# Optimization experiments

Measured on AMD Instinct MI355X. Metric: run time of the kernel, lower is better.

Reference implementation:

```python
import jax, jax.numpy as jnp
import numpy as np

SCALE = 0.1  # FullAttention(0.1) binds scale positionally

def setup_inputs() -> dict:
    key = jax.random.key(0)
    k1, k2, k3, k4, k5 = jax.random.split(key, 5)
    B, H, L, E = 128, 16, 64, 128
    C = H * E  # in_channel = 2048
    return {
        "queries": jax.random.normal(k1, (B, H, L, E), dtype=jnp.float32),
        "keys": jax.random.normal(k2, (B, H, L, E), dtype=jnp.float32),
        "values": jax.random.normal(k3, (B, H, L, E), dtype=jnp.float32),
        "W": jax.random.normal(k4, (C, C), dtype=jnp.float32) * (1.0 / np.sqrt(C)),
        "b": jax.random.normal(k5, (C,), dtype=jnp.float32) * 0.01,
    }

def reference(queries, keys, values, W, b):
    # inputs are [B, H, L, E]; module permutes to [B, L, H, E]
    q = jnp.transpose(queries, (0, 2, 1, 3))  # blhe
    k = jnp.transpose(keys, (0, 2, 1, 3))     # bshe
    v = jnp.transpose(values, (0, 2, 1, 3))   # bshd
    scores = jnp.einsum('blhe,bshe->bhls', q, k)
    A = jax.nn.softmax(SCALE * scores, axis=-1)  # dropout is identity in eval
    V = jnp.einsum('bhls,bshd->blhd', A, v)
    B_, L, H, D = V.shape
    out = V.reshape(-1, 64, H * D)  # view(-1, 64, in_channel)
    return out @ W.T + b
```

## Files before the change

### kernel.cpp

```cpp
#include <hip/hip_runtime.h>
#include <hip/hip_bf16.h>
#include <stdint.h>

typedef __bf16 bf16_t;
typedef __bf16 bf16x4 __attribute__((ext_vector_type(4)));
typedef __bf16 bf16x8 __attribute__((ext_vector_type(8)));
typedef float  f32x4  __attribute__((ext_vector_type(4)));

#define AS1 __attribute__((address_space(1)))
#define AS3 __attribute__((address_space(3)))

__device__ __forceinline__ void gld_lds16(const void* gp, void* lp) {
    __builtin_amdgcn_global_load_lds((const AS1 unsigned int*)gp,
                                     (AS3 unsigned int*)lp, 16, 0, 0);
}

__device__ __forceinline__ bf16_t bhi(float v) { return (bf16_t)v; }
__device__ __forceinline__ bf16_t blo(float v) {
    return (bf16_t)(v - (float)((bf16_t)v));
}

__global__ __launch_bounds__(256) void wconv_kernel(const float* __restrict__ W,
                                                    bf16_t* __restrict__ Wb) {
    const int i = (blockIdx.x * 256 + threadIdx.x) * 4;
    const float4 f = *(const float4*)&W[i];
    bf16x4 v = { (bf16_t)f.x, (bf16_t)f.y, (bf16_t)f.z, (bf16_t)f.w };
    *(bf16x4*)&Wb[i] = v;
}

#define QK_LD 136
#define VT_LD 72
#define SF_LD 65

__global__ __launch_bounds__(256) void attn_kernel(const float* __restrict__ Q,
                                                   const float* __restrict__ K,
                                                   const float* __restrict__ V,
                                                   bf16_t* __restrict__ X) {
    __shared__ __align__(16) char smem[53248];
    bf16_t* Qs = (bf16_t*)smem;
    bf16_t* Ks = (bf16_t*)(smem + 17408);
    bf16_t* Vt = (bf16_t*)(smem + 34816);
    float*  Sf = (float*)smem;
    bf16_t* Ps = (bf16_t*)(smem + 17408);
    bf16_t* Ob = (bf16_t*)smem;

    const int bh   = blockIdx.x;
    const int b    = bh >> 4;
    const int h    = bh & 15;
    const int t    = threadIdx.x;
    const int w    = t >> 6;
    const int lane = t & 63;
    const int row16 = lane & 15;
    const int quad  = lane >> 4;

    const float* Qg = Q + (size_t)bh * 8192;
    const float* Kg = K + (size_t)bh * 8192;
    const float* Vg = V + (size_t)bh * 8192;

    const int r  = t >> 2;
    const int c0 = (t & 3) * 32;

    float qv[32], kv[32];
#pragma unroll
    for (int j = 0; j < 8; ++j) {
        const int c = c0 + 4 * j;
        *(float4*)&qv[4 * j] = *(const float4*)&Qg[r * 128 + c];
        *(float4*)&kv[4 * j] = *(const float4*)&Kg[r * 128 + c];
        const float4 v4 = *(const float4*)&Vg[r * 128 + c];
        Vt[(c + 0) * VT_LD + r] = (bf16_t)v4.x;
        Vt[(c + 1) * VT_LD + r] = (bf16_t)v4.y;
        Vt[(c + 2) * VT_LD + r] = (bf16_t)v4.z;
        Vt[(c + 3) * VT_LD + r] = (bf16_t)v4.w;
    }

#define STAGE(slot, vals, CONV)                                            \
    {                                                                      \
        _Pragma("unroll")                                                  \
        for (int j = 0; j < 8; ++j) {                                      \
            const int c = c0 + 4 * j;                                      \
            bf16x4 o = { CONV(vals[4*j+0]), CONV(vals[4*j+1]),             \
                         CONV(vals[4*j+2]), CONV(vals[4*j+3]) };           \
            *(bf16x4*)&slot[r * QK_LD + c] = o;                            \
        }                                                                  \
    }

    f32x4 accS[4];
#pragma unroll
    for (int ni = 0; ni < 4; ++ni) accS[ni] = (f32x4){0.f, 0.f, 0.f, 0.f};

#define SCORE_PASS()                                                       \
    {                                                                      \
        _Pragma("unroll")                                                  \
        for (int kb = 0; kb < 4; ++kb) {                                   \
            const bf16x8 a = *(const bf16x8*)&Qs[(16*w + row16)*QK_LD + 32*kb + 8*quad]; \
            _Pragma("unroll")                                              \
            for (int ni = 0; ni < 4; ++ni) {                               \
                const bf16x8 bb = *(const bf16x8*)&Ks[(16*ni + row16)*QK_LD + 32*kb + 8*quad]; \
                accS[ni] = __builtin_amdgcn_mfma_f32_16x16x32_bf16(a, bb, accS[ni], 0, 0, 0); \
            }                                                              \
        }                                                                  \
    }

    STAGE(Qs, qv, bhi)
    STAGE(Ks, kv, blo)
    __syncthreads();
    SCORE_PASS()
    __syncthreads();
    STAGE(Ks, kv, bhi)
    __syncthreads();
    SCORE_PASS()
    __syncthreads();
    STAGE(Qs, qv, blo)
    __syncthreads();
    SCORE_PASS()
    __syncthreads();

#pragma unroll
    for (int ni = 0; ni < 4; ++ni)
#pragma unroll
        for (int rr = 0; rr < 4; ++rr)
            Sf[(16 * w + 4 * quad + rr) * SF_LD + 16 * ni + row16] = accS[ni][rr];
    __syncthreads();

    {
        const int c16 = (t & 3) * 16;
        float x[16];
        float mx = -1e30f;
#pragma unroll
        for (int j = 0; j < 16; ++j) {
            x[j] = Sf[r * SF_LD + c16 + j] * 0.1f;
            mx = fmaxf(mx, x[j]);
        }
        mx = fmaxf(mx, __shfl_xor(mx, 1));
        mx = fmaxf(mx, __shfl_xor(mx, 2));
        float sum = 0.f;
#pragma unroll
        for (int j = 0; j < 16; ++j) {
            x[j] = exp2f((x[j] - mx) * 1.44269504088896f);
            sum += x[j];
        }
        sum += __shfl_xor(sum, 1);
        sum += __shfl_xor(sum, 2);
        const float inv = 1.0f / sum;
#pragma unroll
        for (int j4 = 0; j4 < 4; ++j4) {
            bf16x4 p = { (bf16_t)(x[4 * j4 + 0] * inv), (bf16_t)(x[4 * j4 + 1] * inv),
                         (bf16_t)(x[4 * j4 + 2] * inv), (bf16_t)(x[4 * j4 + 3] * inv) };
            *(bf16x4*)&Ps[r * VT_LD + c16 + 4 * j4] = p;
        }
    }
    __syncthreads();

    f32x4 accO[8];
#pragma unroll
    for (int ni = 0; ni < 8; ++ni) accO[ni] = (f32x4){0.f, 0.f, 0.f, 0.f};
#pragma unroll
    for (int kb = 0; kb < 2; ++kb) {
        const bf16x8 a = *(const bf16x8*)&Ps[(16 * w + row16) * VT_LD + 32 * kb + 8 * quad];
#pragma unroll
        for (int ni = 0; ni < 8; ++ni) {
            const bf16x8 bb = *(const bf16x8*)&Vt[(16 * ni + row16) * VT_LD + 32 * kb + 8 * quad];
            accO[ni] = __builtin_amdgcn_mfma_f32_16x16x32_bf16(a, bb, accO[ni], 0, 0, 0);
        }
    }

#pragma unroll
    for (int ni = 0; ni < 8; ++ni)
#pragma unroll
        for (int rr = 0; rr < 4; ++rr)
            Ob[(16 * w + 4 * quad + rr) * QK_LD + 16 * ni + row16] = (bf16_t)accO[ni][rr];
    __syncthreads();

    {
        bf16_t* Xrow = X + (size_t)b * 64 * 2048 + h * 128 + (size_t)r * 2048;
#pragma unroll
        for (int j = 0; j < 4; ++j) {
            *(bf16x8*)&Xrow[c0 + 8 * j] = *(const bf16x8*)&Ob[r * QK_LD + c0 + 8 * j];
        }
    }
}

__global__ __launch_bounds__(256, 4) void gemm_kernel(const bf16_t* __restrict__ X,
                                                      const bf16_t* __restrict__ Wb,
                                                      const float* __restrict__ bias,
                                                      float* __restrict__ out) {
    __shared__ bf16_t As[128 * 64];
    __shared__ bf16_t Bs[128 * 64];

    const int t    = threadIdx.x;
    const int w    = t >> 6;
    const int lane = t & 63;
    const int row16 = lane & 15;
    const int quad  = lane >> 4;
    const int m0 = blockIdx.x * 128;
    const int n0 = blockIdx.y * 128;
    const int wm = w >> 1;
    const int wn = w & 1;

    const int row8 = lane >> 3;
    const int scol = 8 * ((lane & 7) ^ (row8 & 7));
    const bf16_t* gA = X  + (size_t)(m0 + 32 * w + row8) * 2048 + scol;
    const bf16_t* gB = Wb + (size_t)(n0 + 32 * w + row8) * 2048 + scol;
    bf16_t* lA = &As[(32 * w) * 64];
    bf16_t* lB = &Bs[(32 * w) * 64];

    const int sw = row16 & 7;
    int aoff[4][2], boff[4][2];
#pragma unroll
    for (int mi = 0; mi < 4; ++mi)
#pragma unroll
        for (int kk = 0; kk < 2; ++kk) {
            const int ar = 64 * wm + 16 * mi + row16;
            const int br = 64 * wn + 16 * mi + row16;
            aoff[mi][kk] = ar * 64 + 8 * ((4 * kk + quad) ^ sw);
            boff[mi][kk] = br * 64 + 8 * ((4 * kk + quad) ^ sw);
        }

    f32x4 acc[4][4];
#pragma unroll
    for (int mi = 0; mi < 4; ++mi)
#pragma unroll
        for (int ni = 0; ni < 4; ++ni) acc[mi][ni] = (f32x4){0.f, 0.f, 0.f, 0.f};

    for (int kb = 0; kb < 32; ++kb) {
        const int k0 = kb * 64;
        __syncthreads();
#pragma unroll
        for (int i = 0; i < 4; ++i) {
            gld_lds16(gA + (size_t)(8 * i) * 2048 + k0, lA + (8 * i) * 64);
            gld_lds16(gB + (size_t)(8 * i) * 2048 + k0, lB + (8 * i) * 64);
        }
        __syncthreads();

#pragma unroll
        for (int kk = 0; kk < 2; ++kk) {
            bf16x8 a[4], bb[4];
#pragma unroll
            for (int mi = 0; mi < 4; ++mi) a[mi]  = *(const bf16x8*)&As[aoff[mi][kk]];
#pragma unroll
            for (int ni = 0; ni < 4; ++ni) bb[ni] = *(const bf16x8*)&Bs[boff[ni][kk]];
#pragma unroll
            for (int mi = 0; mi < 4; ++mi)
#pragma unroll
                for (int ni = 0; ni < 4; ++ni)
                    acc[mi][ni] = __builtin_amdgcn_mfma_f32_16x16x32_bf16(a[mi], bb[ni], acc[mi][ni], 0, 0, 0);
        }
    }

    const int nb = n0 + 64 * wn;
    float br[4];
#pragma unroll
    for (int ni = 0; ni < 4; ++ni) br[ni] = bias[nb + 16 * ni + row16];
#pragma unroll
    for (int mi = 0; mi < 4; ++mi)
#pragma unroll
        for (int ni = 0; ni < 4; ++ni)
#pragma unroll
            for (int rr = 0; rr < 4; ++rr) {
                const int m = m0 + 64 * wm + 16 * mi + 4 * quad + rr;
                const int n = nb + 16 * ni + row16;
                out[(size_t)m * 2048 + n] = acc[mi][ni][rr] + br[ni];
            }
}

extern "C" void kernel_launch(void* const* d_in, const int* in_sizes, int n_in,
                              void* d_out, int out_size, void* d_ws, size_t ws_size,
                              hipStream_t stream) {
    const float* Q    = (const float*)d_in[0];
    const float* K    = (const float*)d_in[1];
    const float* V    = (const float*)d_in[2];
    const float* W    = (const float*)d_in[3];
    const float* bias = (const float*)d_in[4];

    bf16_t* Xws = (bf16_t*)d_ws;
    bf16_t* Wb  = (bf16_t*)((char*)d_ws + (size_t)8192 * 2048 * 2);
    float*  out = (float*)d_out;

    wconv_kernel<<<4096, 256, 0, stream>>>(W, Wb);
    attn_kernel<<<2048, 256, 0, stream>>>(Q, K, V, Xws);
    gemm_kernel<<<dim3(64, 16), 256, 0, stream>>>(Xws, Wb, bias, out);
}
```

Before: 297.9 us.

## Restructure attention kernel: register Q, swizzled LDS, in-register softmax, fewer barriers

Q is now loaded straight into registers as hi/lo bf16 fragments, and K is split into separate hi and lo LDS buffers. This removes the staged Q/K rewrites and most of the __syncthreads between the three split-precision score passes. Softmax runs on the MFMA accumulators using cross-lane shuffles, which drops the fp32 score round trip through LDS, and normalization is deferred to the output stage. LDS layouts use XOR swizzles instead of padding, and s_setprio hints and a launch bound of 3 are added. The catch is that this only helps the attention kernel, while the GEMM likely dominates total time, and some barriers are replaced by per-wave lgkmcnt waits.

```diff
diff --git a/kernel.cpp b/kernel.cpp
--- a/kernel.cpp
+++ b/kernel.cpp
@@ -28,28 +28,23 @@
     *(bf16x4*)&Wb[i] = v;
 }
 
-#define QK_LD 136
-#define VT_LD 72
-#define SF_LD 65
-
-__global__ __launch_bounds__(256) void attn_kernel(const float* __restrict__ Q,
-                                                   const float* __restrict__ K,
-                                                   const float* __restrict__ V,
-                                                   bf16_t* __restrict__ X) {
-    __shared__ __align__(16) char smem[53248];
-    bf16_t* Qs = (bf16_t*)smem;
-    bf16_t* Ks = (bf16_t*)(smem + 17408);
-    bf16_t* Vt = (bf16_t*)(smem + 34816);
-    float*  Sf = (float*)smem;
-    bf16_t* Ps = (bf16_t*)(smem + 17408);
-    bf16_t* Ob = (bf16_t*)smem;
-
-    const int bh   = blockIdx.x;
-    const int b    = bh >> 4;
-    const int h    = bh & 15;
-    const int t    = threadIdx.x;
-    const int w    = t >> 6;
-    const int lane = t & 63;
+__global__ __launch_bounds__(256, 3) void attn_kernel(const float* __restrict__ Q,
+                                                      const float* __restrict__ K,
+                                                      const float* __restrict__ V,
+                                                      bf16_t* __restrict__ X) {
+    __shared__ __align__(16) char smem[49152];
+    bf16_t* KL = (bf16_t*)smem;
+    bf16_t* KH = (bf16_t*)(smem + 16384);
+    bf16_t* Vt = (bf16_t*)(smem + 32768);
+    bf16_t* Ps = (bf16_t*)smem;
+    bf16_t* Ob = (bf16_t*)(smem + 16384);
+
+    const int bh    = blockIdx.x;
+    const int b     = bh >> 4;
+    const int h     = bh & 15;
+    const int t     = threadIdx.x;
+    const int w     = t >> 6;
+    const int lane  = t & 63;
     const int row16 = lane & 15;
     const int quad  = lane >> 4;
 
@@ -57,125 +52,161 @@
     const float* Kg = K + (size_t)bh * 8192;
     const float* Vg = V + (size_t)bh * 8192;
 
-    const int r  = t >> 2;
-    const int c0 = (t & 3) * 32;
-
-    float qv[32], kv[32];
-#pragma unroll
-    for (int j = 0; j < 8; ++j) {
-        const int c = c0 + 4 * j;
-        *(float4*)&qv[4 * j] = *(const float4*)&Qg[r * 128 + c];
-        *(float4*)&kv[4 * j] = *(const float4*)&Kg[r * 128 + c];
-        const float4 v4 = *(const float4*)&Vg[r * 128 + c];
-        Vt[(c + 0) * VT_LD + r] = (bf16_t)v4.x;
-        Vt[(c + 1) * VT_LD + r] = (bf16_t)v4.y;
-        Vt[(c + 2) * VT_LD + r] = (bf16_t)v4.z;
-        Vt[(c + 3) * VT_LD + r] = (bf16_t)v4.w;
-    }
-
-#define STAGE(slot, vals, CONV)                                            \
-    {                                                                      \
-        _Pragma("unroll")                                                  \
-        for (int j = 0; j < 8; ++j) {                                      \
-            const int c = c0 + 4 * j;                                      \
-            bf16x4 o = { CONV(vals[4*j+0]), CONV(vals[4*j+1]),             \
-                         CONV(vals[4*j+2]), CONV(vals[4*j+3]) };           \
-            *(bf16x4*)&slot[r * QK_LD + c] = o;                            \
-        }                                                                  \
-    }
+    bf16x8 qh8[4], ql8[4];
+    {
+        const float* qrow = Qg + (size_t)(16 * w + row16) * 128 + 8 * quad;
+#pragma unroll
+        for (int kc = 0; kc < 4; ++kc) {
+            const float4 f0 = *(const float4*)&qrow[32 * kc];
+            const float4 f1 = *(const float4*)&qrow[32 * kc + 4];
+            const float f[8] = { f0.x, f0.y, f0.z, f0.w, f1.x, f1.y, f1.z, f1.w };
+            bf16x8 hi, lo;
+#pragma unroll
+            for (int j = 0; j < 8; ++j) {
+                const bf16_t hv = (bf16_t)f[j];
+                hi[j] = hv;
+                lo[j] = (bf16_t)(f[j] - (float)hv);
+            }
+            qh8[kc] = hi;
+            ql8[kc] = lo;
+        }
+    }
+
+    {
+        const int r   = t >> 2;
+        const int c0  = (t & 3) * 32;
+        const int rsw = r & 7;
+#pragma unroll
+        for (int j = 0; j < 8; ++j) {
+            const int c = c0 + 4 * j;
+            const float4 f = *(const float4*)&Kg[r * 128 + c];
+            bf16x4 hi = { bhi(f.x), bhi(f.y), bhi(f.z), bhi(f.w) };
+            bf16x4 lo = { blo(f.x), blo(f.y), blo(f.z), blo(f.w) };
+            const int addr = r * 128 + ((((c >> 3) ^ rsw)) << 3) + (c & 7);
+            *(bf16x4*)&KH[addr] = hi;
+            *(bf16x4*)&KL[addr] = lo;
+        }
+    }
+
+    {
+        const int s = lane;
+#pragma unroll
+        for (int j = 0; j < 8; ++j) {
+            const int d0 = 32 * w + 4 * j;
+            const float4 f = *(const float4*)&Vg[(size_t)s * 128 + d0];
+            const float ff[4] = { f.x, f.y, f.z, f.w };
+#pragma unroll
+            for (int i = 0; i < 4; ++i) {
+                const int d = d0 + i;
+                Vt[d * 64 + ((((s >> 3) ^ (d & 7))) << 3) + (s & 7)] = (bf16_t)ff[i];
+            }
+        }
+    }
+
+    __syncthreads();
 
     f32x4 accS[4];
 #pragma unroll
     for (int ni = 0; ni < 4; ++ni) accS[ni] = (f32x4){0.f, 0.f, 0.f, 0.f};
-
-#define SCORE_PASS()                                                       \
-    {                                                                      \
-        _Pragma("unroll")                                                  \
-        for (int kb = 0; kb < 4; ++kb) {                                   \
-            const bf16x8 a = *(const bf16x8*)&Qs[(16*w + row16)*QK_LD + 32*kb + 8*quad]; \
-            _Pragma("unroll")                                              \
-            for (int ni = 0; ni < 4; ++ni) {                               \
-                const bf16x8 bb = *(const bf16x8*)&Ks[(16*ni + row16)*QK_LD + 32*kb + 8*quad]; \
+    const int bsw = row16 & 7;
+
+#define SPASS(AREG, BS)                                                        \
+    {                                                                          \
+        _Pragma("unroll")                                                      \
+        for (int kc = 0; kc < 4; ++kc) {                                       \
+            const bf16x8 a = AREG[kc];                                         \
+            _Pragma("unroll")                                                  \
+            for (int ni = 0; ni < 4; ++ni) {                                   \
+                const bf16x8 bb = *(const bf16x8*)&BS[(16 * ni + row16) * 128  \
+                                       + ((((4 * kc + quad) ^ bsw)) << 3)];    \
                 accS[ni] = __builtin_amdgcn_mfma_f32_16x16x32_bf16(a, bb, accS[ni], 0, 0, 0); \
-            }                                                              \
-        }                                                                  \
-    }
-
-    STAGE(Qs, qv, bhi)
-    STAGE(Ks, kv, blo)
+            }                                                                  \
+        }                                                                      \
+    }
+
+    __builtin_amdgcn_s_setprio(1);
+    SPASS(qh8, KL)
+    SPASS(qh8, KH)
+    SPASS(ql8, KH)
+    __builtin_amdgcn_s_setprio(0);
+
+    float e[4][4];
+    float inv_[4];
+    const float cs = 0.1f * 1.44269504088896f;
+#pragma unroll
+    for (int rr = 0; rr < 4; ++rr) {
+        float m = fmaxf(fmaxf(accS[0][rr], accS[1][rr]),
+                        fmaxf(accS[2][rr], accS[3][rr]));
+        m = fmaxf(m, __shfl_xor(m, 1));
+        m = fmaxf(m, __shfl_xor(m, 2));
+        m = fmaxf(m, __shfl_xor(m, 4));
+        m = fmaxf(m, __shfl_xor(m, 8));
+        float s0 = 0.f;
+#pragma unroll
+        for (int ni = 0; ni < 4; ++ni) {
+            const float ev = exp2f((accS[ni][rr] - m) * cs);
+            e[ni][rr] = ev;
+            s0 += ev;
+        }
+        s0 += __shfl_xor(s0, 1);
+        s0 += __shfl_xor(s0, 2);
+        s0 += __shfl_xor(s0, 4);
+        s0 += __shfl_xor(s0, 8);
+        inv_[rr] = 1.0f / s0;
+    }
+
     __syncthreads();
-    SCORE_PASS()
-    __syncthreads();
-    STAGE(Ks, kv, bhi)
-    __syncthreads();
-    SCORE_PASS()
-    __syncthreads();
-    STAGE(Qs, qv, blo)
-    __syncthreads();
-    SCORE_PASS()
-    __syncthreads();
-
-#pragma unroll
-    for (int ni = 0; ni < 4; ++ni)
-#pragma unroll
-        for (int rr = 0; rr < 4; ++rr)
-            Sf[(16 * w + 4 * quad + rr) * SF_LD + 16 * ni + row16] = accS[ni][rr];
-    __syncthreads();
+
+#pragma unroll
+    for (int rr = 0; rr < 4; ++rr) {
+        const int l   = 16 * w + 4 * quad + rr;
+        const int lsw = l & 7;
+#pragma unroll
+        for (int ni = 0; ni < 4; ++ni) {
+            const int s = 16 * ni + row16;
+            Ps[l * 64 + ((((s >> 3) ^ lsw)) << 3) + (s & 7)] = (bf16_t)e[ni][rr];
+        }
+    }
+    asm volatile("s_waitcnt lgkmcnt(0)" ::: "memory");
+    __builtin_amdgcn_sched_barrier(0);
+
+    f32x4 accO[8];
+#pragma unroll
+    for (int ni = 0; ni < 8; ++ni) accO[ni] = (f32x4){0.f, 0.f, 0.f, 0.f};
+    __builtin_amdgcn_s_setprio(1);
+#pragma unroll
+    for (int kb = 0; kb < 2; ++kb) {
+        const bf16x8 a = *(const bf16x8*)&Ps[(16 * w + row16) * 64
+                               + ((((4 * kb + quad) ^ bsw)) << 3)];
+#pragma unroll
+        for (int ni = 0; ni < 8; ++ni) {
+            const bf16x8 bb = *(const bf16x8*)&Vt[(16 * ni + row16) * 64
+                                   + ((((4 * kb + quad) ^ bsw)) << 3)];
+            accO[ni] = __builtin_amdgcn_mfma_f32_16x16x32_bf16(a, bb, accO[ni], 0, 0, 0);
+        }
+    }
+    __builtin_amdgcn_s_setprio(0);
+
+#pragma unroll
+    for (int ni = 0; ni < 8; ++ni)
+#pragma unroll
+        for (int rr = 0; rr < 4; ++rr) {
+            const int l = 16 * w + 4 * quad + rr;
+            const int d = 16 * ni + row16;
+            Ob[l * 128 + ((((d >> 3) ^ (5 * rr))) << 3) + (d & 7)] =
+                (bf16_t)(accO[ni][rr] * inv_[rr]);
+        }
+    asm volatile("s_waitcnt lgkmcnt(0)" ::: "memory");
+    __builtin_amdgcn_sched_barrier(0);
 
     {
-        const int c16 = (t & 3) * 16;
-        float x[16];
-        float mx = -1e30f;
-#pragma unroll
-        for (int j = 0; j < 16; ++j) {
-            x[j] = Sf[r * SF_LD + c16 + j] * 0.1f;
-            mx = fmaxf(mx, x[j]);
-        }
-        mx = fmaxf(mx, __shfl_xor(mx, 1));
-        mx = fmaxf(mx, __shfl_xor(mx, 2));
-        float sum = 0.f;
-#pragma unroll
-        for (int j = 0; j < 16; ++j) {
-            x[j] = exp2f((x[j] - mx) * 1.44269504088896f);
-            sum += x[j];
-        }
-        sum += __shfl_xor(sum, 1);
-        sum += __shfl_xor(sum, 2);
-        const float inv = 1.0f / sum;
-#pragma unroll
-        for (int j4 = 0; j4 < 4; ++j4) {
-            bf16x4 p = { (bf16_t)(x[4 * j4 + 0] * inv), (bf16_t)(x[4 * j4 + 1] * inv),
-                         (bf16_t)(x[4 * j4 + 2] * inv), (bf16_t)(x[4 * j4 + 3] * inv) };
-            *(bf16x4*)&Ps[r * VT_LD + c16 + 4 * j4] = p;
-        }
-    }
-    __syncthreads();
-
-    f32x4 accO[8];
-#pragma unroll
-    for (int ni = 0; ni < 8; ++ni) accO[ni] = (f32x4){0.f, 0.f, 0.f, 0.f};
-#pragma unroll
-    for (int kb = 0; kb < 2; ++kb) {
-        const bf16x8 a = *(const bf16x8*)&Ps[(16 * w + row16) * VT_LD + 32 * kb + 8 * quad];
-#pragma unroll
-        for (int ni = 0; ni < 8; ++ni) {
-            const bf16x8 bb = *(const bf16x8*)&Vt[(16 * ni + row16) * VT_LD + 32 * kb + 8 * quad];
-            accO[ni] = __builtin_amdgcn_mfma_f32_16x16x32_bf16(a, bb, accO[ni], 0, 0, 0);
-        }
-    }
-
-#pragma unroll
-    for (int ni = 0; ni < 8; ++ni)
-#pragma unroll
-        for (int rr = 0; rr < 4; ++rr)
-            Ob[(16 * w + 4 * quad + rr) * QK_LD + 16 * ni + row16] = (bf16_t)accO[ni][rr];
-    __syncthreads();
-
-    {
-        bf16_t* Xrow = X + (size_t)b * 64 * 2048 + h * 128 + (size_t)r * 2048;
-#pragma unroll
-        for (int j = 0; j < 4; ++j) {
-            *(bf16x8*)&Xrow[c0 + 8 * j] = *(const bf16x8*)&Ob[r * QK_LD + c0 + 8 * j];
+        const int lr = 16 * w + (lane >> 2);
+        bf16_t* Xrow = X + (size_t)b * 64 * 2048 + h * 128 + (size_t)lr * 2048;
+#pragma unroll
+        for (int jj = 0; jj < 4; ++jj) {
+            const int c8 = (lane & 3) + 4 * jj;
+            const bf16x8 v = *(const bf16x8*)&Ob[lr * 128 + ((c8 ^ (5 * (lr & 3))) << 3)];
+            *(bf16x8*)&Xrow[8 * c8] = v;
         }
     }
 }
```

Measured after the change: 301.3 us. About the same (+1.1%).
